# Optimization experiments

Hardware: AMD Instinct MI355X
Metric: run time of the kernel (lower is better)

## Reference

```python
import jax, jax.numpy as jnp
import numpy as np

GAMMA_MIN = 1e-4
BIG = 1e9  # stands in for +inf; exp(-BIG/gamma) == 0 exactly in fp32, avoids inf-inf NaNs
M, N, D = 4096, 4096, 512


def setup_inputs() -> dict:
    key = jax.random.key(0)
    k1, k2 = jax.random.split(key)
    x = jax.random.normal(k1, (M, D), dtype=jnp.float32)
    y = jax.random.normal(k2, (N, D), dtype=jnp.float32)
    gamma = jnp.asarray(1.0, dtype=jnp.float32)
    return {"x": x, "y": y, "gamma": gamma}


def _softmin(stacked, gamma):
    # softmin over axis 0: -gamma * logsumexp(-v / gamma)
    return -gamma * jax.nn.logsumexp(-stacked / gamma, axis=0)


def _forward_dp(cost, gamma):
    # Anti-diagonal wavefront. diag_d[i] = R[i, d - i] with R (m+1, n+1) DP, R[0,0]=0.
    m, n = cost.shape
    idx = jnp.arange(m + 1)
    diag0 = jnp.full((m + 1,), BIG, cost.dtype).at[0].set(0.0)  # d = 0
    diag1 = jnp.full((m + 1,), BIG, cost.dtype)                 # d = 1 (boundary = inf)

    def step(carry, d):
        prev2, prev1 = carry  # diag_{d-2}, diag_{d-1}
        j = d - idx
        valid = (idx >= 1) & (j >= 1) & (j <= n)
        c = cost[jnp.clip(idx - 1, 0, m - 1), jnp.clip(j - 1, 0, n - 1)]
        p2 = jnp.roll(prev2, 1).at[0].set(BIG)  # R[i-1, j-1]
        p1 = jnp.roll(prev1, 1).at[0].set(BIG)  # R[i-1, j]
        new = jnp.where(valid, c + _softmin(jnp.stack([p2, p1, prev1]), gamma), BIG)
        return (prev1, new), new

    _, diags = jax.lax.scan(step, (diag0, diag1), jnp.arange(2, m + n + 1))
    ii = jnp.arange(1, m + 1)[:, None]
    jj = jnp.arange(1, n + 1)[None, :]
    return diags[ii + jj - 2, ii]  # (m, n): dp_f at cell (i, j)


def _backward_dp(cost, gamma):
    # Reverse DP: E[m,n] = 0; E[i,j] = softmin over reachable successors + cost.
    m, n = cost.shape
    idx = jnp.arange(m + 1)
    diag_top = jnp.full((m + 1,), BIG, cost.dtype)               # d = m+n+1
    diag_mn = jnp.full((m + 1,), BIG, cost.dtype).at[m].set(0.0)  # d = m+n

    def cost_at(i0, j0):
        return cost[jnp.clip(i0, 0, m - 1), jnp.clip(j0, 0, n - 1)]

    def step(carry, d):
        nxt1, nxt2 = carry  # diag_{d+1}, diag_{d+2}
        j = d - idx
        valid = (idx >= 1) & (j >= 1) & (j <= n)
        n1 = jnp.roll(nxt1, -1).at[m].set(BIG)  # E[i+1, j]
        n2 = jnp.roll(nxt2, -1).at[m].set(BIG)  # E[i+1, j+1]
        ok1 = valid & (idx <= m - 1) & (j <= n - 1)
        ok2 = valid & (idx <= m - 1)
        ok3 = valid & (j <= n - 1)
        c1 = jnp.where(ok1, n2 + cost_at(idx, j), BIG)        # diag move
        c2 = jnp.where(ok2, n1 + cost_at(idx, j - 1), BIG)    # down move
        c3 = jnp.where(ok3, nxt1 + cost_at(idx - 1, j), BIG)  # right move
        new = jnp.where(valid, _softmin(jnp.stack([c1, c2, c3]), gamma), BIG)
        new = jnp.where((idx == m) & (j == n), 0.0, new)  # (m,n) stays 0
        return (new, nxt1), new

    _, diags = jax.lax.scan(step, (diag_mn, diag_top), jnp.arange(m + n - 1, 1, -1))
    diags_all = jnp.concatenate([diag_mn[None, :], diags], axis=0)  # row k holds d = m+n-k
    ii = jnp.arange(1, m + 1)[:, None]
    jj = jnp.arange(1, n + 1)[None, :]
    return diags_all[m + n - ii - jj, ii]  # (m, n)


def reference(x, y, gamma):
    g = jnp.maximum(jnp.abs(gamma), GAMMA_MIN)
    xn = x / jnp.maximum(jnp.linalg.norm(x, axis=-1, keepdims=True), 1e-12)
    yn = y / jnp.maximum(jnp.linalg.norm(y, axis=-1, keepdims=True), 1e-12)
    cost = 1.0 - xn @ yn.T  # (M, N) cosine distance
    dp_f = _forward_dp(cost, g)
    distance = dp_f[-1, -1]
    dp_b = _backward_dp(cost, g)
    log_p = jnp.minimum(-(dp_f + cost + dp_b - distance) / g, 0.0)
    alignment = jnp.exp(log_p)
    total = jnp.maximum(alignment.sum(), 1e-8)
    alignment = alignment / total * min(cost.shape)
    return alignment, distance
```

## Files before the change

kernel.cpp:

```cpp
#include <hip/hip_runtime.h>
#include <stdint.h>

#define MDIM 4096
#define NDIM 4096
#define DDIM 512
#define BIGV 1e9f
#define GAMMA_MIN 1e-4f

#define CH 16
#define NSTEPS (NDIM + 63)
#define NCHUNK ((NSTEPS + CH - 1) / CH)

#define LOG2E_F 1.4426950408889634f
#define LN2_F   0.69314718055994531f
#define TAGBASE 0x5A5A0000u

__device__ __forceinline__ float f4c(const float4 v, int j) {
  switch (j & 3) { case 0: return v.x; case 1: return v.y; case 2: return v.z; default: return v.w; }
}
__device__ __forceinline__ float4 ld4u(const float* p) { return *(const float4*)p; }
typedef float f4a __attribute__((ext_vector_type(4), aligned(4)));
__device__ __forceinline__ void st4u(float* p, float a, float b, float c, float d) {
  f4a v = {a, b, c, d};
  *(f4a*)p = v;
}
__device__ __forceinline__ float wshr1o(float old, float x) {
  int r = __builtin_amdgcn_update_dpp(__builtin_bit_cast(int, old),
                                      __builtin_bit_cast(int, x), 0x138, 0xF, 0xF, false);
  return __builtin_bit_cast(float, r);
}
__device__ __forceinline__ uint64_t haloLoad1(const uint64_t* hbase, int col0, int lane) {
  int idx = col0 + (lane & 15);
  if (idx > NDIM - 1) idx = NDIM - 1;
  return __hip_atomic_load(hbase + idx, __ATOMIC_RELAXED, __HIP_MEMORY_SCOPE_AGENT);
}
__device__ __forceinline__ uint64_t haloSpin(const uint64_t* hbase, int col0, int lane,
                                             uint64_t cur) {
  int idx = col0 + (lane & 15);
  if (idx > NDIM - 1) idx = NDIM - 1;
  const uint32_t etag = TAGBASE | (uint32_t)idx;
  while (__ballot((uint32_t)(cur >> 32) == etag) != ~0ull) {
    __builtin_amdgcn_s_sleep(1);
    cur = __hip_atomic_load(hbase + idx, __ATOMIC_RELAXED, __HIP_MEMORY_SCOPE_AGENT);
  }
  return cur;
}
__device__ __forceinline__ void haloUnpack(uint64_t cur, float* hA) {
  const int lo = (int)(uint32_t)(cur & 0xFFFFFFFFull);
#pragma unroll
  for (int s = 0; s < 16; ++s)
    hA[s] = __builtin_bit_cast(float, __builtin_amdgcn_readlane(lo, s));
}
__device__ __forceinline__ void haloStore(uint64_t* hbase, int col, float v) {
  const uint64_t u = ((uint64_t)(TAGBASE | (uint32_t)col) << 32) |
                     (uint64_t)__builtin_bit_cast(uint32_t, v);
  __hip_atomic_store(hbase + col, u, __ATOMIC_RELAXED, __HIP_MEMORY_SCOPE_AGENT);
}

__global__ void init_small(double* __restrict__ sum_p, float* __restrict__ dist_p) {
  if (threadIdx.x == 0) *sum_p = 0.0;
  if (threadIdx.x == 1) *dist_p = 0.0f;
}

__global__ __launch_bounds__(128) void norm_rows(const float* __restrict__ x,
                                                 const float* __restrict__ y,
                                                 float* __restrict__ xn,
                                                 float* __restrict__ yn) {
  const int row = blockIdx.x;
  const float* src = (row < MDIM) ? (x + (size_t)row * DDIM) : (y + (size_t)(row - MDIM) * DDIM);
  float*       dst = (row < MDIM) ? (xn + (size_t)row * DDIM) : (yn + (size_t)(row - MDIM) * DDIM);
  float4 v = ((const float4*)src)[threadIdx.x];
  float ss = v.x * v.x + v.y * v.y + v.z * v.z + v.w * v.w;
#pragma unroll
  for (int off = 32; off > 0; off >>= 1) ss += __shfl_down(ss, off);
  __shared__ float acc[2];
  if ((threadIdx.x & 63) == 0) acc[threadIdx.x >> 6] = ss;
  __syncthreads();
  const float total = acc[0] + acc[1];
  const float inv = 1.0f / fmaxf(sqrtf(total), 1e-12f);
  v.x *= inv; v.y *= inv; v.z *= inv; v.w *= inv;
  ((float4*)dst)[threadIdx.x] = v;
}

#define GT 128
__global__ __launch_bounds__(256) void gemm_cost(const float* __restrict__ xn,
                                                 const float* __restrict__ yn,
                                                 float* __restrict__ cost) {
  __shared__ float As[16][GT + 4];
  __shared__ float Bs[16][GT + 4];
  const int t  = threadIdx.x;
  const int bx = blockIdx.x & 31;
  const int by = blockIdx.x >> 5;
  const int tx = t & 15, ty = t >> 4;
  const int lrow = t >> 1;
  const int lk   = (t & 1) * 8;
  const float* arow = xn + (size_t)(by * GT + lrow) * DDIM + lk;
  const float* brow = yn + (size_t)(bx * GT + lrow) * DDIM + lk;

  float acc[8][8];
#pragma unroll
  for (int i = 0; i < 8; ++i)
#pragma unroll
    for (int j = 0; j < 8; ++j) acc[i][j] = 0.0f;

  for (int kt = 0; kt < DDIM; kt += 16) {
    const float4 a0 = *(const float4*)(arow + kt);
    const float4 a1 = *(const float4*)(arow + kt + 4);
    const float4 b0 = *(const float4*)(brow + kt);
    const float4 b1 = *(const float4*)(brow + kt + 4);
    __syncthreads();
    As[lk + 0][lrow] = a0.x; As[lk + 1][lrow] = a0.y; As[lk + 2][lrow] = a0.z; As[lk + 3][lrow] = a0.w;
    As[lk + 4][lrow] = a1.x; As[lk + 5][lrow] = a1.y; As[lk + 6][lrow] = a1.z; As[lk + 7][lrow] = a1.w;
    Bs[lk + 0][lrow] = b0.x; Bs[lk + 1][lrow] = b0.y; Bs[lk + 2][lrow] = b0.z; Bs[lk + 3][lrow] = b0.w;
    Bs[lk + 4][lrow] = b1.x; Bs[lk + 5][lrow] = b1.y; Bs[lk + 6][lrow] = b1.z; Bs[lk + 7][lrow] = b1.w;
    __syncthreads();
#pragma unroll
    for (int k = 0; k < 16; ++k) {
      const float4 av0 = *(const float4*)&As[k][ty * 8];
      const float4 av1 = *(const float4*)&As[k][ty * 8 + 4];
      const float4 bv0 = *(const float4*)&Bs[k][tx * 8];
      const float4 bv1 = *(const float4*)&Bs[k][tx * 8 + 4];
      const float av[8] = {av0.x, av0.y, av0.z, av0.w, av1.x, av1.y, av1.z, av1.w};
      const float bv[8] = {bv0.x, bv0.y, bv0.z, bv0.w, bv1.x, bv1.y, bv1.z, bv1.w};
#pragma unroll
      for (int i = 0; i < 8; ++i)
#pragma unroll
        for (int j = 0; j < 8; ++j) acc[i][j] = fmaf(av[i], bv[j], acc[i][j]);
    }
  }
#pragma unroll
  for (int i = 0; i < 8; ++i) {
    const size_t row = (size_t)(by * GT + ty * 8 + i);
    float* o = cost + row * NDIM + bx * GT + tx * 8;
    const float4 o0 = make_float4(1.0f - acc[i][0], 1.0f - acc[i][1], 1.0f - acc[i][2], 1.0f - acc[i][3]);
    const float4 o1 = make_float4(1.0f - acc[i][4], 1.0f - acc[i][5], 1.0f - acc[i][6], 1.0f - acc[i][7]);
    *(float4*)o = o0;
    *(float4*)(o + 4) = o1;
  }
}

template <int DIR>
__device__ void run_band(const float* __restrict__ cost, float* __restrict__ dpOut,
                         uint64_t* __restrict__ halo, float* dist_out, float g,
                         int b, int lane) {
  const float k1 = LOG2E_F / g;
  const float k2 = g * LN2_F;
  const int r = b * 64 + lane;
  const float* crow = DIR ? (cost + (size_t)(MDIM - 1 - r) * NDIM + (NDIM - 1))
                          : (cost + (size_t)r * NDIM);
  float* myrow = dpOut + (size_t)r * NDIM;
  uint64_t*       haloW = halo + (size_t)(DIR * 64 + b) * NDIM;
  const uint64_t* haloR = halo + (size_t)(DIR * 64 + b - 1) * NDIM;
  const bool top = (b == 0);
  const bool wr  = (b < 63);

  float v_prev = BIGV;
  float w2 = (top && lane == 0) ? 0.0f : BIGV;
  float vk  = v_prev * k1;
  float w2k = w2 * k1;

  float4 cc[4], cn1[4], cn2[4];
  {
#pragma unroll
    for (int q = 0; q < 4; ++q) {
      const int cb0 = 0 * CH - lane, cb1 = 1 * CH - lane, cb2 = 2 * CH - lane;
      cc[q]  = DIR ? ld4u(crow - cb0 - 4 * q - 3) : ld4u(crow + cb0 + 4 * q);
      cn1[q] = DIR ? ld4u(crow - cb1 - 4 * q - 3) : ld4u(crow + cb1 + 4 * q);
      cn2[q] = DIR ? ld4u(crow - cb2 - 4 * q - 3) : ld4u(crow + cb2 + 4 * q);
    }
  }

  float hA[16];
  uint64_t hB = 0, hC = 0;
  if (!top) {
    uint64_t h0 = haloLoad1(haloR, 0, lane);
    h0 = haloSpin(haloR, 0, lane, h0);
    haloUnpack(h0, hA);
    hB = haloLoad1(haloR, 1 * CH, lane);
    hC = haloLoad1(haloR, 2 * CH, lane);
  }

  for (int c = 0; c < NCHUNK; ++c) {
    float buf[CH];
    const int t0 = c * CH;
    const int base = t0 - lane;
    if (c >= 4 && c <= 255) {
#pragma unroll
      for (int s = 0; s < CH; ++s) {
        const float hold = top ? BIGV : hA[s];
        const float w1 = wshr1o(hold, v_prev);
        const float w1k = w1 * k1;
        const float m = fminf(fminf(w2, w1), v_prev);
        const float e = exp2f(fmaf(m, k1, -w2k)) + exp2f(fmaf(m, k1, -w1k)) +
                        exp2f(fmaf(m, k1, -vk));
        const float cval = DIR ? f4c(cc[s >> 2], 3 - (s & 3)) : f4c(cc[s >> 2], s);
        const float v = fmaf(-k2, log2f(e), m + cval);
        buf[s] = v;
        v_prev = v; vk = v * k1;
        w2 = w1; w2k = w1k;
      }
    } else {
#pragma unroll
      for (int s = 0; s < CH; ++s) {
        const float hold = top ? BIGV : hA[s];
        const float w1 = wshr1o(hold, v_prev);
        const float w1k = w1 * k1;
        const float m = fminf(fminf(w2, w1), v_prev);
        const float e = exp2f(fmaf(m, k1, -w2k)) + exp2f(fmaf(m, k1, -w1k)) +
                        exp2f(fmaf(m, k1, -vk));
        const float cval = DIR ? f4c(cc[s >> 2], 3 - (s & 3)) : f4c(cc[s >> 2], s);
        const float v = fmaf(-k2, log2f(e), m + cval);
        buf[s] = v;
        const bool act = (base + s >= 0) && (base + s < NDIM);
        v_prev = act ? v : v_prev;
        vk     = act ? v * k1 : vk;
        w2 = w1; w2k = w1k;
      }
    }

    if (!top && c + 1 <= 256) {
      hB = haloSpin(haloR, CH * (c + 1), lane, hB);
      haloUnpack(hB, hA);
      hB = hC;
      hC = haloLoad1(haloR, CH * (c + 3), lane);
    }

#pragma unroll
    for (int q = 0; q < 4; ++q) { cc[q] = cn1[q]; cn1[q] = cn2[q]; }
    {
      const int cb = (c + 3) * CH - lane;
#pragma unroll
      for (int q = 0; q < 4; ++q)
        cn2[q] = DIR ? ld4u(crow - cb - 4 * q - 3) : ld4u(crow + cb + 4 * q);
    }

    if (c >= 4 && c <= 255) {
#pragma unroll
      for (int q = 0; q < 4; ++q)
        st4u(myrow + base + 4 * q, buf[4 * q], buf[4 * q + 1], buf[4 * q + 2], buf[4 * q + 3]);
      if (lane == 63 && wr) {
#pragma unroll
        for (int s = 0; s < CH; ++s) haloStore(haloW, base + s, buf[s]);
      }
    } else {
#pragma unroll
      for (int s = 0; s < CH; ++s) {
        const int col = base + s;
        if (col >= 0 && col < NDIM) myrow[col] = buf[s];
      }
      if (lane == 63 && wr) {
#pragma unroll
        for (int s = 0; s < CH; ++s) {
          const int col = base + s;
          if (col >= 0 && col < NDIM) haloStore(haloW, col, buf[s]);
        }
      }
    }
  }
  if (DIR == 0 && b == 63 && lane == 63) *dist_out = v_prev;
}

__global__ __launch_bounds__(64) void dp_kernel(const float* __restrict__ cost,
                                                float* __restrict__ dpF, float* __restrict__ dpG,
                                                uint64_t* __restrict__ halo, float* dist_out,
                                                const float* __restrict__ gamma_p) {
  const int lane = threadIdx.x;
  const float g = fmaxf(fabsf(gamma_p[0]), GAMMA_MIN);
  if (blockIdx.x < 64) run_band<0>(cost, dpF, halo, dist_out, g, blockIdx.x, lane);
  else                 run_band<1>(cost, dpG, halo, dist_out, g, blockIdx.x - 64, lane);
}

__global__ __launch_bounds__(256) void pass1(float* __restrict__ out, const float* __restrict__ dpG,
                                             const float* __restrict__ dist_p,
                                             const float* __restrict__ gamma_p,
                                             double* __restrict__ sum_p) {
  const size_t idx4 = (size_t)blockIdx.x * 256 + threadIdx.x;
  const size_t base = idx4 * 4;
  const float g = fmaxf(fabsf(gamma_p[0]), GAMMA_MIN);
  const float invg = 1.0f / g;
  const float dist = *dist_p;
  const float4 f = ((const float4*)out)[idx4];
  const float4 grev = ((const float4*)dpG)[(16777212u - base) >> 2];
  const float x0 = fminf((dist - f.x - grev.w) * invg, 0.0f);
  const float x1 = fminf((dist - f.y - grev.z) * invg, 0.0f);
  const float x2 = fminf((dist - f.z - grev.y) * invg, 0.0f);
  const float x3 = fminf((dist - f.w - grev.x) * invg, 0.0f);
  const float a0 = exp2f(x0 * LOG2E_F), a1 = exp2f(x1 * LOG2E_F);
  const float a2 = exp2f(x2 * LOG2E_F), a3 = exp2f(x3 * LOG2E_F);
  ((float4*)out)[idx4] = make_float4(a0, a1, a2, a3);
  float s = a0 + a1 + a2 + a3;
#pragma unroll
  for (int off = 32; off > 0; off >>= 1) s += __shfl_down(s, off);
  __shared__ float wsum[4];
  if ((threadIdx.x & 63) == 0) wsum[threadIdx.x >> 6] = s;
  __syncthreads();
  if (threadIdx.x == 0) atomicAdd(sum_p, (double)(wsum[0] + wsum[1] + wsum[2] + wsum[3]));
}

__global__ __launch_bounds__(256) void pass2(float* __restrict__ out,
                                             const double* __restrict__ sum_p,
                                             const float* __restrict__ dist_p) {
  const size_t idx4 = (size_t)blockIdx.x * 256 + threadIdx.x;
  const float total = fmaxf((float)*sum_p, 1e-8f);
  const float scale = 4096.0f / total;
  float4 v = ((const float4*)out)[idx4];
  v.x *= scale; v.y *= scale; v.z *= scale; v.w *= scale;
  ((float4*)out)[idx4] = v;
  if (idx4 == 0) out[16777216] = *dist_p;
}

extern "C" void kernel_launch(void* const* d_in, const int* in_sizes, int n_in,
                              void* d_out, int out_size, void* d_ws, size_t ws_size,
                              hipStream_t stream) {
  const float* x = (const float*)d_in[0];
  const float* y = (const float*)d_in[1];
  const float* gamma_p = (const float*)d_in[2];
  float* out = (float*)d_out;

  uint8_t* w = (uint8_t*)d_ws;
  const size_t SZ_MAT = (size_t)MDIM * NDIM * sizeof(float);
  const size_t SZ_XN  = (size_t)MDIM * DDIM * sizeof(float);
  float* xn  = (float*)w;
  float* yn  = (float*)(w + SZ_XN);
  float* dpG = (float*)w;
  float* cost = (float*)(w + SZ_MAT + 512);
  uint8_t* small = w + SZ_MAT + 512 + SZ_MAT + 512;
  double* sum_p  = (double*)small;
  float*  dist_p = (float*)(small + 8);
  uint64_t* halo = (uint64_t*)d_in[0];

  hipLaunchKernelGGL(init_small, dim3(1), dim3(64), 0, stream, sum_p, dist_p);
  hipLaunchKernelGGL(norm_rows, dim3(2 * MDIM), dim3(128), 0, stream, x, y, xn, yn);
  hipLaunchKernelGGL(gemm_cost, dim3((MDIM / GT) * (NDIM / GT)), dim3(256), 0, stream, xn, yn, cost);
  hipLaunchKernelGGL(dp_kernel, dim3(128), dim3(64), 0, stream, cost, out, dpG, halo, dist_p, gamma_p);
  hipLaunchKernelGGL(pass1, dim3(MDIM * NDIM / 1024), dim3(256), 0, stream, out, dpG, dist_p, gamma_p, sum_p);
  hipLaunchKernelGGL(pass2, dim3(MDIM * NDIM / 1024), dim3(256), 0, stream, out, sum_p, dist_p);
}
```

Before: 2.294 ms.

## Group four DP bands per workgroup and pass halos through LDS with flags

Packs four consecutive 64-row wavefront bands into one 256-thread workgroup. Bands inside a workgroup hand off their boundary row through shared memory guarded by LDS flags. Only the band at each workgroup edge still uses the tagged global halo with spin-waiting. This is meant to cut global atomic halo latency on the serial wavefront critical path. In exchange, four waves now share one CU and there are only 32 workgroups, so compute may contend within the CU, and LDS ordering relies on s_waitcnt plus relaxed atomics.

```diff
diff --git a/kernel.cpp b/kernel.cpp
--- a/kernel.cpp
+++ b/kernel.cpp
@@ -10,6 +10,8 @@
 #define CH 16
 #define NSTEPS (NDIM + 63)
 #define NCHUNK ((NSTEPS + CH - 1) / CH)
+#define WPB 4
+#define NBR 16
 
 #define LOG2E_F 1.4426950408889634f
 #define LN2_F   0.69314718055994531f
@@ -55,6 +57,12 @@
   const uint64_t u = ((uint64_t)(TAGBASE | (uint32_t)col) << 32) |
                      (uint64_t)__builtin_bit_cast(uint32_t, v);
   __hip_atomic_store(hbase + col, u, __ATOMIC_RELAXED, __HIP_MEMORY_SCOPE_AGENT);
+}
+__device__ __forceinline__ int ldsFlagLoad(const int* p) {
+  return __hip_atomic_load(p, __ATOMIC_RELAXED, __HIP_MEMORY_SCOPE_WORKGROUP);
+}
+__device__ __forceinline__ void ldsFlagStore(int* p, int v) {
+  __hip_atomic_store(p, v, __ATOMIC_RELAXED, __HIP_MEMORY_SCOPE_WORKGROUP);
 }
 
 __global__ void init_small(double* __restrict__ sum_p, float* __restrict__ dist_p) {
@@ -142,17 +150,22 @@
 template <int DIR>
 __device__ void run_band(const float* __restrict__ cost, float* __restrict__ dpOut,
                          uint64_t* __restrict__ halo, float* dist_out, float g,
-                         int b, int lane) {
+                         int br, int w, int lane,
+                         float* lhaloR, float* lhaloW, int* flagR, int* flagW) {
   const float k1 = LOG2E_F / g;
   const float k2 = g * LN2_F;
+  const int b = br * WPB + w;
   const int r = b * 64 + lane;
   const float* crow = DIR ? (cost + (size_t)(MDIM - 1 - r) * NDIM + (NDIM - 1))
                           : (cost + (size_t)r * NDIM);
   float* myrow = dpOut + (size_t)r * NDIM;
-  uint64_t*       haloW = halo + (size_t)(DIR * 64 + b) * NDIM;
-  const uint64_t* haloR = halo + (size_t)(DIR * 64 + b - 1) * NDIM;
-  const bool top = (b == 0);
-  const bool wr  = (b < 63);
+  const bool top   = (b == 0);
+  const bool ldsR  = (w > 0);
+  const bool globR = (!top && !ldsR);
+  const bool ldsW  = (w < WPB - 1);
+  const bool globW = (!ldsW && br < NBR - 1);
+  const uint64_t* ghR = halo + (size_t)(DIR * NBR + (br > 0 ? br - 1 : 0)) * NDIM;
+  uint64_t*       ghW = halo + (size_t)(DIR * NBR + br) * NDIM;
 
   float v_prev = BIGV;
   float w2 = (top && lane == 0) ? 0.0f : BIGV;
@@ -160,24 +173,31 @@
   float w2k = w2 * k1;
 
   float4 cc[4], cn1[4], cn2[4];
-  {
-#pragma unroll
-    for (int q = 0; q < 4; ++q) {
-      const int cb0 = 0 * CH - lane, cb1 = 1 * CH - lane, cb2 = 2 * CH - lane;
-      cc[q]  = DIR ? ld4u(crow - cb0 - 4 * q - 3) : ld4u(crow + cb0 + 4 * q);
-      cn1[q] = DIR ? ld4u(crow - cb1 - 4 * q - 3) : ld4u(crow + cb1 + 4 * q);
-      cn2[q] = DIR ? ld4u(crow - cb2 - 4 * q - 3) : ld4u(crow + cb2 + 4 * q);
-    }
+#pragma unroll
+  for (int q = 0; q < 4; ++q) {
+    const int cb0 = 0 * CH - lane, cb1 = 1 * CH - lane, cb2 = 2 * CH - lane;
+    cc[q]  = DIR ? ld4u(crow - cb0 - 4 * q - 3) : ld4u(crow + cb0 + 4 * q);
+    cn1[q] = DIR ? ld4u(crow - cb1 - 4 * q - 3) : ld4u(crow + cb1 + 4 * q);
+    cn2[q] = DIR ? ld4u(crow - cb2 - 4 * q - 3) : ld4u(crow + cb2 + 4 * q);
   }
 
   float hA[16];
   uint64_t hB = 0, hC = 0;
-  if (!top) {
-    uint64_t h0 = haloLoad1(haloR, 0, lane);
-    h0 = haloSpin(haloR, 0, lane, h0);
+  if (globR) {
+    uint64_t h0 = haloLoad1(ghR, 0, lane);
+    h0 = haloSpin(ghR, 0, lane, h0);
     haloUnpack(h0, hA);
-    hB = haloLoad1(haloR, 1 * CH, lane);
-    hC = haloLoad1(haloR, 2 * CH, lane);
+    hB = haloLoad1(ghR, 1 * CH, lane);
+    hC = haloLoad1(ghR, 2 * CH, lane);
+  } else if (ldsR) {
+    while (ldsFlagLoad(flagR) < 5) __builtin_amdgcn_s_sleep(1);
+    asm volatile("" ::: "memory");
+    const float4* lp = (const float4*)&lhaloR[0];
+#pragma unroll
+    for (int q = 0; q < 4; ++q) {
+      const float4 hv = lp[q];
+      hA[4 * q] = hv.x; hA[4 * q + 1] = hv.y; hA[4 * q + 2] = hv.z; hA[4 * q + 3] = hv.w;
+    }
   }
 
   for (int c = 0; c < NCHUNK; ++c) {
@@ -218,11 +238,22 @@
       }
     }
 
-    if (!top && c + 1 <= 256) {
-      hB = haloSpin(haloR, CH * (c + 1), lane, hB);
+    if (globR && c + 1 <= 256) {
+      hB = haloSpin(ghR, CH * (c + 1), lane, hB);
       haloUnpack(hB, hA);
       hB = hC;
-      hC = haloLoad1(haloR, CH * (c + 3), lane);
+      hC = haloLoad1(ghR, CH * (c + 3), lane);
+    } else if (ldsR && c + 1 <= 255) {
+      int need = c + 6;
+      if (need > NCHUNK) need = NCHUNK;
+      while (ldsFlagLoad(flagR) < need) __builtin_amdgcn_s_sleep(1);
+      asm volatile("" ::: "memory");
+      const float4* lp = (const float4*)&lhaloR[CH * (c + 1)];
+#pragma unroll
+      for (int q = 0; q < 4; ++q) {
+        const float4 hv = lp[q];
+        hA[4 * q] = hv.x; hA[4 * q + 1] = hv.y; hA[4 * q + 2] = hv.z; hA[4 * q + 3] = hv.w;
+      }
     }
 
 #pragma unroll
@@ -238,21 +269,37 @@
 #pragma unroll
       for (int q = 0; q < 4; ++q)
         st4u(myrow + base + 4 * q, buf[4 * q], buf[4 * q + 1], buf[4 * q + 2], buf[4 * q + 3]);
-      if (lane == 63 && wr) {
-#pragma unroll
-        for (int s = 0; s < CH; ++s) haloStore(haloW, base + s, buf[s]);
-      }
     } else {
 #pragma unroll
       for (int s = 0; s < CH; ++s) {
         const int col = base + s;
         if (col >= 0 && col < NDIM) myrow[col] = buf[s];
       }
-      if (lane == 63 && wr) {
+    }
+    if (ldsW) {
+      if (lane == 63) {
+        if (c >= 4 && c <= 255) {
+#pragma unroll
+          for (int s = 0; s < CH; ++s) lhaloW[base + s] = buf[s];
+        } else {
+#pragma unroll
+          for (int s = 0; s < CH; ++s) {
+            const int col = base + s;
+            if (col >= 0 && col < NDIM) lhaloW[col] = buf[s];
+          }
+        }
+      }
+      asm volatile("s_waitcnt lgkmcnt(0)" ::: "memory");
+      if (lane == 63) ldsFlagStore(flagW, c + 1);
+    } else if (globW && lane == 63) {
+      if (c >= 4 && c <= 255) {
+#pragma unroll
+        for (int s = 0; s < CH; ++s) haloStore(ghW, base + s, buf[s]);
+      } else {
 #pragma unroll
         for (int s = 0; s < CH; ++s) {
           const int col = base + s;
-          if (col >= 0 && col < NDIM) haloStore(haloW, col, buf[s]);
+          if (col >= 0 && col < NDIM) haloStore(ghW, col, buf[s]);
         }
       }
     }
@@ -260,14 +307,24 @@
   if (DIR == 0 && b == 63 && lane == 63) *dist_out = v_prev;
 }
 
-__global__ __launch_bounds__(64) void dp_kernel(const float* __restrict__ cost,
-                                                float* __restrict__ dpF, float* __restrict__ dpG,
-                                                uint64_t* __restrict__ halo, float* dist_out,
-                                                const float* __restrict__ gamma_p) {
-  const int lane = threadIdx.x;
+__global__ __launch_bounds__(256) void dp_kernel(const float* __restrict__ cost,
+                                                 float* __restrict__ dpF, float* __restrict__ dpG,
+                                                 uint64_t* __restrict__ halo, float* dist_out,
+                                                 const float* __restrict__ gamma_p) {
+  __shared__ float lh[WPB - 1][NDIM];
+  __shared__ int   lf[WPB - 1];
+  const int w = threadIdx.x >> 6, lane = threadIdx.x & 63;
+  if (threadIdx.x < WPB - 1) lf[threadIdx.x] = 0;
+  __syncthreads();
+  const int dir = blockIdx.x >> 4;
+  const int br  = blockIdx.x & 15;
   const float g = fmaxf(fabsf(gamma_p[0]), GAMMA_MIN);
-  if (blockIdx.x < 64) run_band<0>(cost, dpF, halo, dist_out, g, blockIdx.x, lane);
-  else                 run_band<1>(cost, dpG, halo, dist_out, g, blockIdx.x - 64, lane);
+  float* lhR = (w > 0) ? lh[w - 1] : nullptr;
+  float* lhW = (w < WPB - 1) ? lh[w] : nullptr;
+  int* fR = (w > 0) ? &lf[w - 1] : nullptr;
+  int* fW = (w < WPB - 1) ? &lf[w] : nullptr;
+  if (dir == 0) run_band<0>(cost, dpF, halo, dist_out, g, br, w, lane, lhR, lhW, fR, fW);
+  else          run_band<1>(cost, dpG, halo, dist_out, g, br, w, lane, lhR, lhW, fR, fW);
 }
 
 __global__ __launch_bounds__(256) void pass1(float* __restrict__ out, const float* __restrict__ dpG,
@@ -332,7 +389,7 @@
   hipLaunchKernelGGL(init_small, dim3(1), dim3(64), 0, stream, sum_p, dist_p);
   hipLaunchKernelGGL(norm_rows, dim3(2 * MDIM), dim3(128), 0, stream, x, y, xn, yn);
   hipLaunchKernelGGL(gemm_cost, dim3((MDIM / GT) * (NDIM / GT)), dim3(256), 0, stream, xn, yn, cost);
-  hipLaunchKernelGGL(dp_kernel, dim3(128), dim3(64), 0, stream, cost, out, dpG, halo, dist_p, gamma_p);
+  hipLaunchKernelGGL(dp_kernel, dim3(2 * NBR), dim3(64 * WPB), 0, stream, cost, out, dpG, halo, dist_p, gamma_p);
   hipLaunchKernelGGL(pass1, dim3(MDIM * NDIM / 1024), dim3(256), 0, stream, out, dpG, dist_p, gamma_p, sum_p);
   hipLaunchKernelGGL(pass2, dim3(MDIM * NDIM / 1024), dim3(256), 0, stream, out, sum_p, dist_p);
 }
```

After: 2.051 ms. -10.6%, faster.
